# Optimization experiments

Hardware: AMD Instinct MI355X
Metric: run time of the kernel (lower is better)

Reference implementation:

```python
import jax, jax.numpy as jnp
import numpy as np

N = 100000          # active sites
C_IN = 256          # inplanes == outplanes
C_MID = 64          # innerplanes
K = 9               # 3x3 kernel offsets (2D)


def setup_inputs() -> dict:
    key = jax.random.key(0)
    ks = jax.random.split(key, 12)
    features = jax.random.normal(ks[0], (N, C_IN), dtype=jnp.float32)
    # submanifold rulebook: for each active site, index of active neighbor per
    # kernel offset; sentinel N = no active neighbor, center (offset 4) = self
    idx = jax.random.randint(ks[1], (N, K), 0, N, dtype=jnp.int32)
    drop = jax.random.uniform(ks[2], (N, K)) < 0.3
    idx = jnp.where(drop, jnp.int32(N), idx)
    neighbor_idx = idx.at[:, 4].set(jnp.arange(N, dtype=jnp.int32))
    s = 0.05
    return {
        "features": features,
        "neighbor_idx": neighbor_idx,
        "w1": jax.random.normal(ks[3], (C_IN, C_MID), dtype=jnp.float32) * s,
        "scale1": jnp.ones((C_MID,), jnp.float32),
        "bias1": jnp.zeros((C_MID,), jnp.float32),
        "w2": jax.random.normal(ks[4], (K, C_MID, C_MID), dtype=jnp.float32) * s,
        "scale2": jnp.ones((C_MID,), jnp.float32),
        "bias2": jnp.zeros((C_MID,), jnp.float32),
        "w3": jax.random.normal(ks[5], (C_MID, C_IN), dtype=jnp.float32) * s,
        "scale3": jnp.ones((C_IN,), jnp.float32),
        "bias3": jnp.zeros((C_IN,), jnp.float32),
    }


def reference(features, neighbor_idx, w1, scale1, bias1, w2, scale2, bias2,
              w3, scale3, bias3):
    # conv1: 1x1 submanifold conv == per-site matmul; affine BN; ReLU
    out = jax.nn.relu(features @ w1 * scale1 + bias1)            # [N, C_MID]
    # conv2: 3x3 submanifold conv via rulebook gather-matmul-accumulate
    padded = jnp.concatenate([out, jnp.zeros((1, C_MID), out.dtype)], axis=0)
    gathered = padded[neighbor_idx]                               # [N, K, C_MID]
    out = jnp.einsum('nkc,kcd->nd', gathered, w2)                 # [N, C_MID]
    out = jax.nn.relu(out * scale2 + bias2)
    # conv3: 1x1 conv; affine BN; residual add (downsample=None); ReLU
    out = out @ w3 * scale3 + bias3 + features                    # [N, C_IN]
    return jax.nn.relu(out)
```

## Files before the change

### kernel.cpp

```cpp
#include <hip/hip_runtime.h>
#include <stdint.h>

#define C_IN 256
#define C_MID 64
#define KOFF 9

typedef __attribute__((ext_vector_type(8))) short bf16x8;
typedef __attribute__((ext_vector_type(4))) short short4v;
typedef __attribute__((ext_vector_type(4))) float f32x4;
typedef __attribute__((ext_vector_type(4))) float float4v;

__device__ inline unsigned short f2bf(float f) {
    union { float f; unsigned u; } x; x.f = f;
    unsigned r = x.u + 0x7FFFu + ((x.u >> 16) & 1u);
    return (unsigned short)(r >> 16);
}

__global__ void prep_kernel(const float* __restrict__ w1, const float* __restrict__ s1,
                            const float* __restrict__ w2, const float* __restrict__ s2,
                            const float* __restrict__ w3, const float* __restrict__ s3,
                            unsigned short* __restrict__ w1t,
                            unsigned short* __restrict__ w2t,
                            unsigned short* __restrict__ w3t,
                            unsigned short* __restrict__ zrow) {
    int tid = blockIdx.x * blockDim.x + threadIdx.x;
    int stride = gridDim.x * blockDim.x;
    for (int i = tid; i < C_MID * C_IN; i += stride) {
        int n = i / C_IN, k = i % C_IN;
        w1t[i] = f2bf(w1[k * C_MID + n] * s1[n]);
    }
    for (int i = tid; i < KOFF * C_MID * C_MID; i += stride) {
        int k = i / (C_MID * C_MID);
        int r = i % (C_MID * C_MID);
        int d = r / C_MID, c = r % C_MID;
        w2t[i] = f2bf(w2[(k * C_MID + c) * C_MID + d] * s2[d]);
    }
    for (int i = tid; i < C_IN * C_MID; i += stride) {
        int e = i / C_MID, c = i % C_MID;
        w3t[i] = f2bf(w3[c * C_IN + e] * s3[e]);
    }
    for (int i = tid; i < C_MID; i += stride) zrow[i] = 0;
}

__global__ __launch_bounds__(256, 4) void conv1_kernel(
    const float* __restrict__ feat, const unsigned short* __restrict__ w1t,
    const float* __restrict__ b1, unsigned short* __restrict__ out1, int N)
{
    __shared__ __align__(16) unsigned short sW1[16384];

    int t = threadIdx.x;
    int wave = t >> 6;
    int lane = t & 63;
    int l15 = lane & 15;
    int quad = lane >> 4;
    int site = blockIdx.x * 64 + wave * 16 + l15;
    int sitec = site < N ? site : (N - 1);

    const bf16x8* w1c = reinterpret_cast<const bf16x8*>(w1t);
    bf16x8* sW1c = reinterpret_cast<bf16x8*>(sW1);
#pragma unroll
    for (int it = 0; it < 8; ++it) {
        int s = it * 256 + t;
        int l = s & 15, ct = (s >> 4) & 3, q = (s >> 6) & 3, kk = s >> 8;
        sW1c[s] = w1c[(ct * 16 + l) * 32 + kk * 4 + q];
    }

    float4v fr0[8];
#pragma unroll
    for (int kk = 0; kk < 4; ++kk) {
        const float4v* p = reinterpret_cast<const float4v*>(
            feat + (size_t)sitec * C_IN + kk * 32 + quad * 8);
        fr0[kk * 2] = p[0];
        fr0[kk * 2 + 1] = p[1];
    }
    __builtin_amdgcn_sched_barrier(0);
    __syncthreads();

    float4v fr1[8];
#pragma unroll
    for (int kk = 0; kk < 4; ++kk) {
        const float4v* p = reinterpret_cast<const float4v*>(
            feat + (size_t)sitec * C_IN + (kk + 4) * 32 + quad * 8);
        fr1[kk * 2] = p[0];
        fr1[kk * 2 + 1] = p[1];
    }
    __builtin_amdgcn_sched_barrier(0);

    f32x4 acc[4] = {};
#pragma unroll
    for (int kk = 0; kk < 4; ++kk) {
        union { unsigned short s[8]; bf16x8 v; } ua;
#pragma unroll
        for (int j = 0; j < 4; ++j) {
            ua.s[j] = f2bf(fr0[kk * 2][j]);
            ua.s[4 + j] = f2bf(fr0[kk * 2 + 1][j]);
        }
#pragma unroll
        for (int ct = 0; ct < 4; ++ct) {
            bf16x8 fa = sW1c[((kk * 4 + quad) * 4 + ct) * 16 + l15];
            acc[ct] = __builtin_amdgcn_mfma_f32_16x16x32_bf16(fa, ua.v, acc[ct], 0, 0, 0);
        }
    }
#pragma unroll
    for (int kk = 0; kk < 4; ++kk) {
        union { unsigned short s[8]; bf16x8 v; } ua;
#pragma unroll
        for (int j = 0; j < 4; ++j) {
            ua.s[j] = f2bf(fr1[kk * 2][j]);
            ua.s[4 + j] = f2bf(fr1[kk * 2 + 1][j]);
        }
#pragma unroll
        for (int ct = 0; ct < 4; ++ct) {
            bf16x8 fa = sW1c[(((kk + 4) * 4 + quad) * 4 + ct) * 16 + l15];
            acc[ct] = __builtin_amdgcn_mfma_f32_16x16x32_bf16(fa, ua.v, acc[ct], 0, 0, 0);
        }
    }
    if (site < N) {
#pragma unroll
        for (int ct = 0; ct < 4; ++ct) {
            float4v bb = *reinterpret_cast<const float4v*>(b1 + ct * 16 + quad * 4);
            union { unsigned short s[4]; short4v v; } o;
#pragma unroll
            for (int reg = 0; reg < 4; ++reg)
                o.s[reg] = f2bf(fmaxf(acc[ct][reg] + bb[reg], 0.f));
            *reinterpret_cast<short4v*>(out1 + (size_t)site * C_MID + ct * 16 + quad * 4) = o.v;
        }
    }
}

__global__ __launch_bounds__(256, 2) void conv23_kernel(
    const float* __restrict__ feat, const int* __restrict__ nbr,
    const unsigned short* __restrict__ out1, const unsigned short* __restrict__ w2t,
    const float* __restrict__ b2, const unsigned short* __restrict__ w3t,
    const float* __restrict__ b3, float* __restrict__ out, int N)
{
    __shared__ __align__(16) unsigned short sWB[21504];
    __shared__ int sNbr[64 * KOFF];

    int t = threadIdx.x;
    int wave = t >> 6;
    int lane = t & 63;
    int l15 = lane & 15;
    int quad = lane >> 4;
    int rt = wave * 16 + l15;
    int site = blockIdx.x * 64 + rt;
    int sitec = site < N ? site : (N - 1);

    bf16x8* sWBc = reinterpret_cast<bf16x8*>(sWB);
    const bf16x8* w2c = reinterpret_cast<const bf16x8*>(w2t);

#pragma unroll
    for (int it = 0; it < 10; ++it) {
        int s = it * 256 + t;
        int l = s & 15, ct = (s >> 4) & 3, q = (s >> 6) & 3, kk = (s >> 8) & 1, k = s >> 9;
        sWBc[s] = w2c[k * 512 + (ct * 16 + l) * 8 + kk * 4 + q];
    }
#pragma unroll
    for (int i = 0; i < 3; ++i) {
        int j = i * 256 + t;
        if (j < 64 * KOFF) {
            int g = blockIdx.x * 64 * KOFF + j;
            sNbr[j] = (g < N * KOFF) ? nbr[g] : N;
        }
    }
    __syncthreads();

    int nb[KOFF];
#pragma unroll
    for (int k = 0; k < KOFF; ++k) nb[k] = sNbr[rt * KOFF + k];

    bf16x8 ga[KOFF][2];
#pragma unroll
    for (int k = 0; k < KOFF; ++k) {
        const bf16x8* pg = reinterpret_cast<const bf16x8*>(out1 + (size_t)nb[k] * C_MID + quad * 8);
        ga[k][0] = pg[0];
        ga[k][1] = pg[4];
    }
    __builtin_amdgcn_sched_barrier(0);

    f32x4 acc2[4] = {};
#pragma unroll
    for (int k = 0; k < 5; ++k) {
#pragma unroll
        for (int kk = 0; kk < 2; ++kk) {
#pragma unroll
            for (int ct = 0; ct < 4; ++ct) {
                bf16x8 fa = sWBc[((k * 2 + kk) * 4 + quad) * 64 + ct * 16 + l15];
                acc2[ct] = __builtin_amdgcn_mfma_f32_16x16x32_bf16(fa, ga[k][kk], acc2[ct], 0, 0, 0);
            }
        }
    }
    __syncthreads();

#pragma unroll
    for (int it = 0; it < 8; ++it) {
        int s = it * 256 + t;
        int l = s & 15, ct = (s >> 4) & 3, q = (s >> 6) & 3, kk = (s >> 8) & 1, k2 = s >> 9;
        sWBc[s] = w2c[(5 + k2) * 512 + (ct * 16 + l) * 8 + kk * 4 + q];
    }
    __syncthreads();
#pragma unroll
    for (int k = 5; k < KOFF; ++k) {
        int kloc = k - 5;
#pragma unroll
        for (int kk = 0; kk < 2; ++kk) {
#pragma unroll
            for (int ct = 0; ct < 4; ++ct) {
                bf16x8 fa = sWBc[((kloc * 2 + kk) * 4 + quad) * 64 + ct * 16 + l15];
                acc2[ct] = __builtin_amdgcn_mfma_f32_16x16x32_bf16(fa, ga[k][kk], acc2[ct], 0, 0, 0);
            }
        }
    }
    float4v rf[16];
#pragma unroll
    for (int c2 = 0; c2 < 16; ++c2)
        rf[c2] = *reinterpret_cast<const float4v*>(
            feat + (size_t)sitec * C_IN + c2 * 16 + quad * 4);
    __builtin_amdgcn_sched_barrier(0);
    __syncthreads();

    unsigned short* mid = &sWB[16384];
#pragma unroll
    for (int ct = 0; ct < 4; ++ct) {
        float4v bb = *reinterpret_cast<const float4v*>(b2 + ct * 16 + quad * 4);
        union { unsigned short s[4]; short4v v; } o;
#pragma unroll
        for (int reg = 0; reg < 4; ++reg)
            o.s[reg] = f2bf(fmaxf(acc2[ct][reg] + bb[reg], 0.f));
        *reinterpret_cast<short4v*>(&mid[rt * 72 + ct * 16 + quad * 4]) = o.v;
    }
    const bf16x8* w3c = reinterpret_cast<const bf16x8*>(w3t);
#pragma unroll
    for (int it = 0; it < 8; ++it) {
        int s = it * 256 + t;
        int l = s & 15, c2 = (s >> 4) & 15, q = (s >> 8) & 3, kk = (s >> 10) & 1;
        sWBc[s] = w3c[(c2 * 16 + l) * 8 + kk * 4 + q];
    }
    __syncthreads();

    f32x4 acc3[16] = {};
#pragma unroll
    for (int kk = 0; kk < 2; ++kk) {
        bf16x8 fb = *reinterpret_cast<const bf16x8*>(
            &mid[rt * 72 + kk * 32 + quad * 8]);
#pragma unroll
        for (int c2 = 0; c2 < 16; ++c2) {
            bf16x8 fa = sWBc[((kk * 4 + quad) * 16 + c2) * 16 + l15];
            acc3[c2] = __builtin_amdgcn_mfma_f32_16x16x32_bf16(fa, fb, acc3[c2], 0, 0, 0);
        }
    }
    if (site < N) {
#pragma unroll
        for (int c2 = 0; c2 < 16; ++c2) {
            float4v bb = *reinterpret_cast<const float4v*>(b3 + c2 * 16 + quad * 4);
            float4v o;
#pragma unroll
            for (int reg = 0; reg < 4; ++reg)
                o[reg] = fmaxf(acc3[c2][reg] + bb[reg] + rf[c2][reg], 0.f);
            *reinterpret_cast<float4v*>(out + (size_t)site * C_IN + c2 * 16 + quad * 4) = o;
        }
    }
}

extern "C" void kernel_launch(void* const* d_in, const int* in_sizes, int n_in,
                              void* d_out, int out_size, void* d_ws, size_t ws_size,
                              hipStream_t stream) {
    const float* feat = (const float*)d_in[0];
    const int*   nbr  = (const int*)d_in[1];
    const float* w1   = (const float*)d_in[2];
    const float* s1   = (const float*)d_in[3];
    const float* b1   = (const float*)d_in[4];
    const float* w2   = (const float*)d_in[5];
    const float* s2   = (const float*)d_in[6];
    const float* b2   = (const float*)d_in[7];
    const float* w3   = (const float*)d_in[8];
    const float* s3   = (const float*)d_in[9];
    const float* b3   = (const float*)d_in[10];
    float* out = (float*)d_out;
    int N = in_sizes[0] / C_IN;

    char* ws = (char*)d_ws;
    unsigned short* w1t  = (unsigned short*)(ws);
    unsigned short* w2t  = (unsigned short*)(ws + 32768);
    unsigned short* w3t  = (unsigned short*)(ws + 32768 + 73728);
    unsigned short* out1 = (unsigned short*)(ws + 139264);

    prep_kernel<<<80, 256, 0, stream>>>(w1, s1, w2, s2, w3, s3, w1t, w2t, w3t,
                                        out1 + (size_t)N * C_MID);
    int nblk = (N + 63) / 64;
    conv1_kernel<<<nblk, 256, 0, stream>>>(feat, w1t, b1, out1, N);
    conv23_kernel<<<nblk, 256, 0, stream>>>(feat, nbr, out1, w2t, b2, w3t, b3, out, N);
}
```

Baseline: 260.7 us.

## Read weights directly from global/L2 instead of staging in LDS; raise conv23 occupancy

Removes the LDS weight-staging loops and their barriers in both conv1 and conv23, so each lane loads MFMA weight fragments straight from global memory, where they should hit cache. conv23 now keeps only the small mid buffer in shared memory, raises launch bounds to 4 blocks per CU, and computes the conv3 output in four chunks of four column tiles to cut accumulator registers. The aim is to drop per-block weight copy and sync overhead and gain occupancy for latency hiding. The cost is more scattered global loads per MFMA operand, which rely on L1/L2 hit rates.

```diff
diff --git a/kernel.cpp b/kernel.cpp
--- a/kernel.cpp
+++ b/kernel.cpp
@@ -46,8 +46,6 @@
     const float* __restrict__ feat, const unsigned short* __restrict__ w1t,
     const float* __restrict__ b1, unsigned short* __restrict__ out1, int N)
 {
-    __shared__ __align__(16) unsigned short sW1[16384];
-
     int t = threadIdx.x;
     int wave = t >> 6;
     int lane = t & 63;
@@ -57,61 +55,29 @@
     int sitec = site < N ? site : (N - 1);
 
     const bf16x8* w1c = reinterpret_cast<const bf16x8*>(w1t);
-    bf16x8* sW1c = reinterpret_cast<bf16x8*>(sW1);
-#pragma unroll
-    for (int it = 0; it < 8; ++it) {
-        int s = it * 256 + t;
-        int l = s & 15, ct = (s >> 4) & 3, q = (s >> 6) & 3, kk = s >> 8;
-        sW1c[s] = w1c[(ct * 16 + l) * 32 + kk * 4 + q];
-    }
-
-    float4v fr0[8];
-#pragma unroll
-    for (int kk = 0; kk < 4; ++kk) {
+
+    float4v fr[16];
+#pragma unroll
+    for (int kk = 0; kk < 8; ++kk) {
         const float4v* p = reinterpret_cast<const float4v*>(
             feat + (size_t)sitec * C_IN + kk * 32 + quad * 8);
-        fr0[kk * 2] = p[0];
-        fr0[kk * 2 + 1] = p[1];
+        fr[kk * 2] = p[0];
+        fr[kk * 2 + 1] = p[1];
     }
     __builtin_amdgcn_sched_barrier(0);
-    __syncthreads();
-
-    float4v fr1[8];
-#pragma unroll
-    for (int kk = 0; kk < 4; ++kk) {
-        const float4v* p = reinterpret_cast<const float4v*>(
-            feat + (size_t)sitec * C_IN + (kk + 4) * 32 + quad * 8);
-        fr1[kk * 2] = p[0];
-        fr1[kk * 2 + 1] = p[1];
-    }
-    __builtin_amdgcn_sched_barrier(0);
 
     f32x4 acc[4] = {};
 #pragma unroll
-    for (int kk = 0; kk < 4; ++kk) {
+    for (int kk = 0; kk < 8; ++kk) {
         union { unsigned short s[8]; bf16x8 v; } ua;
 #pragma unroll
         for (int j = 0; j < 4; ++j) {
-            ua.s[j] = f2bf(fr0[kk * 2][j]);
-            ua.s[4 + j] = f2bf(fr0[kk * 2 + 1][j]);
+            ua.s[j] = f2bf(fr[kk * 2][j]);
+            ua.s[4 + j] = f2bf(fr[kk * 2 + 1][j]);
         }
 #pragma unroll
         for (int ct = 0; ct < 4; ++ct) {
-            bf16x8 fa = sW1c[((kk * 4 + quad) * 4 + ct) * 16 + l15];
-            acc[ct] = __builtin_amdgcn_mfma_f32_16x16x32_bf16(fa, ua.v, acc[ct], 0, 0, 0);
-        }
-    }
-#pragma unroll
-    for (int kk = 0; kk < 4; ++kk) {
-        union { unsigned short s[8]; bf16x8 v; } ua;
-#pragma unroll
-        for (int j = 0; j < 4; ++j) {
-            ua.s[j] = f2bf(fr1[kk * 2][j]);
-            ua.s[4 + j] = f2bf(fr1[kk * 2 + 1][j]);
-        }
-#pragma unroll
-        for (int ct = 0; ct < 4; ++ct) {
-            bf16x8 fa = sW1c[(((kk + 4) * 4 + quad) * 4 + ct) * 16 + l15];
+            bf16x8 fa = w1c[(ct * 16 + l15) * 32 + kk * 4 + quad];
             acc[ct] = __builtin_amdgcn_mfma_f32_16x16x32_bf16(fa, ua.v, acc[ct], 0, 0, 0);
         }
     }
@@ -128,13 +94,13 @@
     }
 }
 
-__global__ __launch_bounds__(256, 2) void conv23_kernel(
+__global__ __launch_bounds__(256, 4) void conv23_kernel(
     const float* __restrict__ feat, const int* __restrict__ nbr,
     const unsigned short* __restrict__ out1, const unsigned short* __restrict__ w2t,
     const float* __restrict__ b2, const unsigned short* __restrict__ w3t,
     const float* __restrict__ b3, float* __restrict__ out, int N)
 {
-    __shared__ __align__(16) unsigned short sWB[21504];
+    __shared__ __align__(16) unsigned short mid[64 * 72];
     __shared__ int sNbr[64 * KOFF];
 
     int t = threadIdx.x;
@@ -146,15 +112,6 @@
     int site = blockIdx.x * 64 + rt;
     int sitec = site < N ? site : (N - 1);
 
-    bf16x8* sWBc = reinterpret_cast<bf16x8*>(sWB);
-    const bf16x8* w2c = reinterpret_cast<const bf16x8*>(w2t);
-
-#pragma unroll
-    for (int it = 0; it < 10; ++it) {
-        int s = it * 256 + t;
-        int l = s & 15, ct = (s >> 4) & 3, q = (s >> 6) & 3, kk = (s >> 8) & 1, k = s >> 9;
-        sWBc[s] = w2c[k * 512 + (ct * 16 + l) * 8 + kk * 4 + q];
-    }
 #pragma unroll
     for (int i = 0; i < 3; ++i) {
         int j = i * 256 + t;
@@ -178,86 +135,64 @@
     }
     __builtin_amdgcn_sched_barrier(0);
 
+    const bf16x8* w2c = reinterpret_cast<const bf16x8*>(w2t);
     f32x4 acc2[4] = {};
 #pragma unroll
-    for (int k = 0; k < 5; ++k) {
+    for (int k = 0; k < KOFF; ++k) {
 #pragma unroll
         for (int kk = 0; kk < 2; ++kk) {
 #pragma unroll
             for (int ct = 0; ct < 4; ++ct) {
-                bf16x8 fa = sWBc[((k * 2 + kk) * 4 + quad) * 64 + ct * 16 + l15];
+                bf16x8 fa = w2c[k * 512 + (ct * 16 + l15) * 8 + kk * 4 + quad];
                 acc2[ct] = __builtin_amdgcn_mfma_f32_16x16x32_bf16(fa, ga[k][kk], acc2[ct], 0, 0, 0);
             }
         }
     }
+
+#pragma unroll
+    for (int ct = 0; ct < 4; ++ct) {
+        float4v bb = *reinterpret_cast<const float4v*>(b2 + ct * 16 + quad * 4);
+        union { unsigned short s[4]; short4v v; } o;
+#pragma unroll
+        for (int reg = 0; reg < 4; ++reg)
+            o.s[reg] = f2bf(fmaxf(acc2[ct][reg] + bb[reg], 0.f));
+        *reinterpret_cast<short4v*>(&mid[rt * 72 + ct * 16 + quad * 4]) = o.v;
+    }
     __syncthreads();
 
-#pragma unroll
-    for (int it = 0; it < 8; ++it) {
-        int s = it * 256 + t;
-        int l = s & 15, ct = (s >> 4) & 3, q = (s >> 6) & 3, kk = (s >> 8) & 1, k2 = s >> 9;
-        sWBc[s] = w2c[(5 + k2) * 512 + (ct * 16 + l) * 8 + kk * 4 + q];
-    }
-    __syncthreads();
-#pragma unroll
-    for (int k = 5; k < KOFF; ++k) {
-        int kloc = k - 5;
-#pragma unroll
-        for (int kk = 0; kk < 2; ++kk) {
-#pragma unroll
-            for (int ct = 0; ct < 4; ++ct) {
-                bf16x8 fa = sWBc[((kloc * 2 + kk) * 4 + quad) * 64 + ct * 16 + l15];
-                acc2[ct] = __builtin_amdgcn_mfma_f32_16x16x32_bf16(fa, ga[k][kk], acc2[ct], 0, 0, 0);
-            }
-        }
-    }
     float4v rf[16];
 #pragma unroll
     for (int c2 = 0; c2 < 16; ++c2)
         rf[c2] = *reinterpret_cast<const float4v*>(
             feat + (size_t)sitec * C_IN + c2 * 16 + quad * 4);
     __builtin_amdgcn_sched_barrier(0);
-    __syncthreads();
-
-    unsigned short* mid = &sWB[16384];
-#pragma unroll
-    for (int ct = 0; ct < 4; ++ct) {
-        float4v bb = *reinterpret_cast<const float4v*>(b2 + ct * 16 + quad * 4);
-        union { unsigned short s[4]; short4v v; } o;
-#pragma unroll
-        for (int reg = 0; reg < 4; ++reg)
-            o.s[reg] = f2bf(fmaxf(acc2[ct][reg] + bb[reg], 0.f));
-        *reinterpret_cast<short4v*>(&mid[rt * 72 + ct * 16 + quad * 4]) = o.v;
-    }
+
     const bf16x8* w3c = reinterpret_cast<const bf16x8*>(w3t);
 #pragma unroll
-    for (int it = 0; it < 8; ++it) {
-        int s = it * 256 + t;
-        int l = s & 15, c2 = (s >> 4) & 15, q = (s >> 8) & 3, kk = (s >> 10) & 1;
-        sWBc[s] = w3c[(c2 * 16 + l) * 8 + kk * 4 + q];
-    }
-    __syncthreads();
-
-    f32x4 acc3[16] = {};
-#pragma unroll
-    for (int kk = 0; kk < 2; ++kk) {
-        bf16x8 fb = *reinterpret_cast<const bf16x8*>(
-            &mid[rt * 72 + kk * 32 + quad * 8]);
-#pragma unroll
-        for (int c2 = 0; c2 < 16; ++c2) {
-            bf16x8 fa = sWBc[((kk * 4 + quad) * 16 + c2) * 16 + l15];
-            acc3[c2] = __builtin_amdgcn_mfma_f32_16x16x32_bf16(fa, fb, acc3[c2], 0, 0, 0);
-        }
-    }
-    if (site < N) {
-#pragma unroll
-        for (int c2 = 0; c2 < 16; ++c2) {
-            float4v bb = *reinterpret_cast<const float4v*>(b3 + c2 * 16 + quad * 4);
-            float4v o;
-#pragma unroll
-            for (int reg = 0; reg < 4; ++reg)
-                o[reg] = fmaxf(acc3[c2][reg] + bb[reg] + rf[c2][reg], 0.f);
-            *reinterpret_cast<float4v*>(out + (size_t)site * C_IN + c2 * 16 + quad * 4) = o;
+    for (int c = 0; c < 4; ++c) {
+        f32x4 acc3[4] = {};
+#pragma unroll
+        for (int kk = 0; kk < 2; ++kk) {
+            bf16x8 fb = *reinterpret_cast<const bf16x8*>(
+                &mid[rt * 72 + kk * 32 + quad * 8]);
+#pragma unroll
+            for (int c2l = 0; c2l < 4; ++c2l) {
+                int c2 = c * 4 + c2l;
+                bf16x8 fa = w3c[(c2 * 16 + l15) * 8 + kk * 4 + quad];
+                acc3[c2l] = __builtin_amdgcn_mfma_f32_16x16x32_bf16(fa, fb, acc3[c2l], 0, 0, 0);
+            }
+        }
+        if (site < N) {
+#pragma unroll
+            for (int c2l = 0; c2l < 4; ++c2l) {
+                int c2 = c * 4 + c2l;
+                float4v bb = *reinterpret_cast<const float4v*>(b3 + c2 * 16 + quad * 4);
+                float4v o;
+#pragma unroll
+                for (int reg = 0; reg < 4; ++reg)
+                    o[reg] = fmaxf(acc3[c2l][reg] + bb[reg] + rf[c2][reg], 0.f);
+                *reinterpret_cast<float4v*>(out + (size_t)site * C_IN + c2 * 16 + quad * 4) = o;
+            }
         }
     }
 }
```

New measurement: 326.1 us. 25.1% more time.

## Split fused conv2/conv3 kernel into separate kernels via bf16 mid buffer

Applied to the files above, without the earlier changes.

Replaces the fused conv23 kernel with a conv2 kernel that writes the bf16 intermediate to workspace and a conv3 kernel that reads it back, when the workspace is large enough. Each kernel uses less LDS and fewer registers, so it targets higher occupancy (launch bounds of 3 blocks per CU) and better latency hiding for the gathers and the residual loads. conv2 streams its weights in three stages, and conv3 stores its output in chunks of four tiles to cut live accumulators. The cost is an extra global round trip for the mid tensor (about 12.8MB written and read) plus one more kernel launch.

```diff
diff --git a/kernel.cpp b/kernel.cpp
--- a/kernel.cpp
+++ b/kernel.cpp
@@ -128,6 +128,180 @@
     }
 }
 
+__global__ __launch_bounds__(256, 3) void conv2_kernel(
+    const int* __restrict__ nbr, const unsigned short* __restrict__ out1,
+    const unsigned short* __restrict__ w2t, const float* __restrict__ b2,
+    unsigned short* __restrict__ mid, int N)
+{
+    __shared__ __align__(16) unsigned short sW2[12288];
+    __shared__ int sNbr[64 * KOFF];
+
+    int t = threadIdx.x;
+    int wave = t >> 6;
+    int lane = t & 63;
+    int l15 = lane & 15;
+    int quad = lane >> 4;
+    int rt = wave * 16 + l15;
+    int site = blockIdx.x * 64 + rt;
+
+    bf16x8* sW2c = reinterpret_cast<bf16x8*>(sW2);
+    const bf16x8* w2c = reinterpret_cast<const bf16x8*>(w2t);
+
+#pragma unroll
+    for (int it = 0; it < 6; ++it) {
+        int s = it * 256 + t;
+        int l = s & 15, ct = (s >> 4) & 3, q = (s >> 6) & 3, kk = (s >> 8) & 1, k2 = s >> 9;
+        sW2c[s] = w2c[k2 * 512 + (ct * 16 + l) * 8 + kk * 4 + q];
+    }
+#pragma unroll
+    for (int i = 0; i < 3; ++i) {
+        int j = i * 256 + t;
+        if (j < 64 * KOFF) {
+            int g = blockIdx.x * 64 * KOFF + j;
+            sNbr[j] = (g < N * KOFF) ? nbr[g] : N;
+        }
+    }
+    __syncthreads();
+
+    int nb[KOFF];
+#pragma unroll
+    for (int k = 0; k < KOFF; ++k) nb[k] = sNbr[rt * KOFF + k];
+
+    bf16x8 ga[KOFF][2];
+#pragma unroll
+    for (int k = 0; k < KOFF; ++k) {
+        const bf16x8* pg = reinterpret_cast<const bf16x8*>(out1 + (size_t)nb[k] * C_MID + quad * 8);
+        ga[k][0] = pg[0];
+        ga[k][1] = pg[4];
+    }
+    __builtin_amdgcn_sched_barrier(0);
+
+    f32x4 acc2[4] = {};
+#pragma unroll
+    for (int k2 = 0; k2 < 3; ++k2) {
+#pragma unroll
+        for (int kk = 0; kk < 2; ++kk) {
+#pragma unroll
+            for (int ct = 0; ct < 4; ++ct) {
+                bf16x8 fa = sW2c[((k2 * 2 + kk) * 4 + quad) * 64 + ct * 16 + l15];
+                acc2[ct] = __builtin_amdgcn_mfma_f32_16x16x32_bf16(fa, ga[k2][kk], acc2[ct], 0, 0, 0);
+            }
+        }
+    }
+    __syncthreads();
+
+#pragma unroll
+    for (int it = 0; it < 6; ++it) {
+        int s = it * 256 + t;
+        int l = s & 15, ct = (s >> 4) & 3, q = (s >> 6) & 3, kk = (s >> 8) & 1, k2 = s >> 9;
+        sW2c[s] = w2c[(3 + k2) * 512 + (ct * 16 + l) * 8 + kk * 4 + q];
+    }
+    __syncthreads();
+#pragma unroll
+    for (int k2 = 0; k2 < 3; ++k2) {
+#pragma unroll
+        for (int kk = 0; kk < 2; ++kk) {
+#pragma unroll
+            for (int ct = 0; ct < 4; ++ct) {
+                bf16x8 fa = sW2c[((k2 * 2 + kk) * 4 + quad) * 64 + ct * 16 + l15];
+                acc2[ct] = __builtin_amdgcn_mfma_f32_16x16x32_bf16(fa, ga[3 + k2][kk], acc2[ct], 0, 0, 0);
+            }
+        }
+    }
+    __syncthreads();
+
+#pragma unroll
+    for (int it = 0; it < 6; ++it) {
+        int s = it * 256 + t;
+        int l = s & 15, ct = (s >> 4) & 3, q = (s >> 6) & 3, kk = (s >> 8) & 1, k2 = s >> 9;
+        sW2c[s] = w2c[(6 + k2) * 512 + (ct * 16 + l) * 8 + kk * 4 + q];
+    }
+    __syncthreads();
+#pragma unroll
+    for (int k2 = 0; k2 < 3; ++k2) {
+#pragma unroll
+        for (int kk = 0; kk < 2; ++kk) {
+#pragma unroll
+            for (int ct = 0; ct < 4; ++ct) {
+                bf16x8 fa = sW2c[((k2 * 2 + kk) * 4 + quad) * 64 + ct * 16 + l15];
+                acc2[ct] = __builtin_amdgcn_mfma_f32_16x16x32_bf16(fa, ga[6 + k2][kk], acc2[ct], 0, 0, 0);
+            }
+        }
+    }
+
+    if (site < N) {
+#pragma unroll
+        for (int ct = 0; ct < 4; ++ct) {
+            float4v bb = *reinterpret_cast<const float4v*>(b2 + ct * 16 + quad * 4);
+            union { unsigned short s[4]; short4v v; } o;
+#pragma unroll
+            for (int reg = 0; reg < 4; ++reg)
+                o.s[reg] = f2bf(fmaxf(acc2[ct][reg] + bb[reg], 0.f));
+            *reinterpret_cast<short4v*>(mid + (size_t)site * C_MID + ct * 16 + quad * 4) = o.v;
+        }
+    }
+}
+
+__global__ __launch_bounds__(256, 3) void conv3_kernel(
+    const float* __restrict__ feat, const unsigned short* __restrict__ mid,
+    const unsigned short* __restrict__ w3t, const float* __restrict__ b3,
+    float* __restrict__ out, int N)
+{
+    __shared__ __align__(16) unsigned short sW3[16384];
+
+    int t = threadIdx.x;
+    int wave = t >> 6;
+    int lane = t & 63;
+    int l15 = lane & 15;
+    int quad = lane >> 4;
+    int site = blockIdx.x * 64 + wave * 16 + l15;
+    int sitec = site < N ? site : (N - 1);
+
+    bf16x8* sW3c = reinterpret_cast<bf16x8*>(sW3);
+    const bf16x8* w3c = reinterpret_cast<const bf16x8*>(w3t);
+#pragma unroll
+    for (int it = 0; it < 8; ++it) {
+        int s = it * 256 + t;
+        int l = s & 15, c2 = (s >> 4) & 15, q = (s >> 8) & 3, kk = (s >> 10) & 1;
+        sW3c[s] = w3c[(c2 * 16 + l) * 8 + kk * 4 + q];
+    }
+
+    bf16x8 fb0 = *reinterpret_cast<const bf16x8*>(mid + (size_t)sitec * C_MID + quad * 8);
+    bf16x8 fb1 = *reinterpret_cast<const bf16x8*>(mid + (size_t)sitec * C_MID + 32 + quad * 8);
+    float4v rf[16];
+#pragma unroll
+    for (int c2 = 0; c2 < 16; ++c2)
+        rf[c2] = *reinterpret_cast<const float4v*>(
+            feat + (size_t)sitec * C_IN + c2 * 16 + quad * 4);
+    __builtin_amdgcn_sched_barrier(0);
+    __syncthreads();
+
+#pragma unroll
+    for (int c = 0; c < 4; ++c) {
+        f32x4 acc3[4] = {};
+#pragma unroll
+        for (int c2l = 0; c2l < 4; ++c2l) {
+            int c2 = c * 4 + c2l;
+            bf16x8 fa0 = sW3c[((0 * 4 + quad) * 16 + c2) * 16 + l15];
+            acc3[c2l] = __builtin_amdgcn_mfma_f32_16x16x32_bf16(fa0, fb0, acc3[c2l], 0, 0, 0);
+            bf16x8 fa1 = sW3c[((1 * 4 + quad) * 16 + c2) * 16 + l15];
+            acc3[c2l] = __builtin_amdgcn_mfma_f32_16x16x32_bf16(fa1, fb1, acc3[c2l], 0, 0, 0);
+        }
+        if (site < N) {
+#pragma unroll
+            for (int c2l = 0; c2l < 4; ++c2l) {
+                int c2 = c * 4 + c2l;
+                float4v bb = *reinterpret_cast<const float4v*>(b3 + c2 * 16 + quad * 4);
+                float4v o;
+#pragma unroll
+                for (int reg = 0; reg < 4; ++reg)
+                    o[reg] = fmaxf(acc3[c2l][reg] + bb[reg] + rf[c2][reg], 0.f);
+                *reinterpret_cast<float4v*>(out + (size_t)site * C_IN + c2 * 16 + quad * 4) = o;
+            }
+        }
+    }
+}
+
 __global__ __launch_bounds__(256, 2) void conv23_kernel(
     const float* __restrict__ feat, const int* __restrict__ nbr,
     const unsigned short* __restrict__ out1, const unsigned short* __restrict__ w2t,
@@ -219,7 +393,7 @@
     __builtin_amdgcn_sched_barrier(0);
     __syncthreads();
 
-    unsigned short* mid = &sWB[16384];
+    unsigned short* midl = &sWB[16384];
 #pragma unroll
     for (int ct = 0; ct < 4; ++ct) {
         float4v bb = *reinterpret_cast<const float4v*>(b2 + ct * 16 + quad * 4);
@@ -227,7 +401,7 @@
 #pragma unroll
         for (int reg = 0; reg < 4; ++reg)
             o.s[reg] = f2bf(fmaxf(acc2[ct][reg] + bb[reg], 0.f));
-        *reinterpret_cast<short4v*>(&mid[rt * 72 + ct * 16 + quad * 4]) = o.v;
+        *reinterpret_cast<short4v*>(&midl[rt * 72 + ct * 16 + quad * 4]) = o.v;
     }
     const bf16x8* w3c = reinterpret_cast<const bf16x8*>(w3t);
 #pragma unroll
@@ -242,7 +416,7 @@
 #pragma unroll
     for (int kk = 0; kk < 2; ++kk) {
         bf16x8 fb = *reinterpret_cast<const bf16x8*>(
-            &mid[rt * 72 + kk * 32 + quad * 8]);
+            &midl[rt * 72 + kk * 32 + quad * 8]);
 #pragma unroll
         for (int c2 = 0; c2 < 16; ++c2) {
             bf16x8 fa = sWBc[((kk * 4 + quad) * 16 + c2) * 16 + l15];
@@ -285,9 +459,19 @@
     unsigned short* w3t  = (unsigned short*)(ws + 32768 + 73728);
     unsigned short* out1 = (unsigned short*)(ws + 139264);
 
+    size_t out1_bytes = (size_t)(N + 1) * C_MID * 2;
+    size_t need_split = 139264 + out1_bytes + (size_t)N * C_MID * 2;
+
     prep_kernel<<<80, 256, 0, stream>>>(w1, s1, w2, s2, w3, s3, w1t, w2t, w3t,
                                         out1 + (size_t)N * C_MID);
     int nblk = (N + 63) / 64;
     conv1_kernel<<<nblk, 256, 0, stream>>>(feat, w1t, b1, out1, N);
-    conv23_kernel<<<nblk, 256, 0, stream>>>(feat, nbr, out1, w2t, b2, w3t, b3, out, N);
-}
+
+    if (ws_size >= need_split) {
+        unsigned short* mid = (unsigned short*)(ws + 139264 + out1_bytes);
+        conv2_kernel<<<nblk, 256, 0, stream>>>(nbr, out1, w2t, b2, mid, N);
+        conv3_kernel<<<nblk, 256, 0, stream>>>(feat, mid, w3t, b3, out, N);
+    } else {
+        conv23_kernel<<<nblk, 256, 0, stream>>>(feat, nbr, out1, w2t, b2, w3t, b3, out, N);
+    }
+}
```

Result: slower. 266.7 us (+2.3%).

## Shrink conv23 LDS footprint to fit three blocks per CU

Applied to the files above, without the earlier changes.

Splits the w2 weight staging into three phases of three offsets, so the shared buffer shrinks from about 43KB to about 35KB with a separate mid buffer. The w3 operands are now read directly from global memory (L2-cached) instead of being staged in LDS. The conv3 output is produced in four column chunks of four accumulators each, which cuts live registers. Together with launch_bounds(256,3) this aims to raise occupancy and hide gather latency, at the cost of extra barriers and global weight loads per wave.

```diff
diff --git a/kernel.cpp b/kernel.cpp
--- a/kernel.cpp
+++ b/kernel.cpp
@@ -128,13 +128,14 @@
     }
 }
 
-__global__ __launch_bounds__(256, 2) void conv23_kernel(
+__global__ __launch_bounds__(256, 3) void conv23_kernel(
     const float* __restrict__ feat, const int* __restrict__ nbr,
     const unsigned short* __restrict__ out1, const unsigned short* __restrict__ w2t,
     const float* __restrict__ b2, const unsigned short* __restrict__ w3t,
     const float* __restrict__ b3, float* __restrict__ out, int N)
 {
-    __shared__ __align__(16) unsigned short sWB[21504];
+    __shared__ __align__(16) unsigned short sW2[12288];
+    __shared__ __align__(16) unsigned short sMid[64 * 72];
     __shared__ int sNbr[64 * KOFF];
 
     int t = threadIdx.x;
@@ -146,14 +147,14 @@
     int site = blockIdx.x * 64 + rt;
     int sitec = site < N ? site : (N - 1);
 
-    bf16x8* sWBc = reinterpret_cast<bf16x8*>(sWB);
+    bf16x8* sW2c = reinterpret_cast<bf16x8*>(sW2);
     const bf16x8* w2c = reinterpret_cast<const bf16x8*>(w2t);
 
 #pragma unroll
-    for (int it = 0; it < 10; ++it) {
+    for (int it = 0; it < 6; ++it) {
         int s = it * 256 + t;
-        int l = s & 15, ct = (s >> 4) & 3, q = (s >> 6) & 3, kk = (s >> 8) & 1, k = s >> 9;
-        sWBc[s] = w2c[k * 512 + (ct * 16 + l) * 8 + kk * 4 + q];
+        int l = s & 15, ct = (s >> 4) & 3, q = (s >> 6) & 3, kk = (s >> 8) & 1, k2 = s >> 9;
+        sW2c[s] = w2c[k2 * 512 + (ct * 16 + l) * 8 + kk * 4 + q];
     }
 #pragma unroll
     for (int i = 0; i < 3; ++i) {
@@ -180,37 +181,67 @@
 
     f32x4 acc2[4] = {};
 #pragma unroll
-    for (int k = 0; k < 5; ++k) {
+    for (int k2 = 0; k2 < 3; ++k2) {
 #pragma unroll
         for (int kk = 0; kk < 2; ++kk) {
 #pragma unroll
             for (int ct = 0; ct < 4; ++ct) {
-                bf16x8 fa = sWBc[((k * 2 + kk) * 4 + quad) * 64 + ct * 16 + l15];
-                acc2[ct] = __builtin_amdgcn_mfma_f32_16x16x32_bf16(fa, ga[k][kk], acc2[ct], 0, 0, 0);
+                bf16x8 fa = sW2c[((k2 * 2 + kk) * 4 + quad) * 64 + ct * 16 + l15];
+                acc2[ct] = __builtin_amdgcn_mfma_f32_16x16x32_bf16(fa, ga[k2][kk], acc2[ct], 0, 0, 0);
             }
         }
     }
     __syncthreads();
 
 #pragma unroll
-    for (int it = 0; it < 8; ++it) {
+    for (int it = 0; it < 6; ++it) {
         int s = it * 256 + t;
         int l = s & 15, ct = (s >> 4) & 3, q = (s >> 6) & 3, kk = (s >> 8) & 1, k2 = s >> 9;
-        sWBc[s] = w2c[(5 + k2) * 512 + (ct * 16 + l) * 8 + kk * 4 + q];
-    }
-    __syncthreads();
-#pragma unroll
-    for (int k = 5; k < KOFF; ++k) {
-        int kloc = k - 5;
+        sW2c[s] = w2c[(3 + k2) * 512 + (ct * 16 + l) * 8 + kk * 4 + q];
+    }
+    __syncthreads();
+#pragma unroll
+    for (int k2 = 0; k2 < 3; ++k2) {
 #pragma unroll
         for (int kk = 0; kk < 2; ++kk) {
 #pragma unroll
             for (int ct = 0; ct < 4; ++ct) {
-                bf16x8 fa = sWBc[((kloc * 2 + kk) * 4 + quad) * 64 + ct * 16 + l15];
-                acc2[ct] = __builtin_amdgcn_mfma_f32_16x16x32_bf16(fa, ga[k][kk], acc2[ct], 0, 0, 0);
+                bf16x8 fa = sW2c[((k2 * 2 + kk) * 4 + quad) * 64 + ct * 16 + l15];
+                acc2[ct] = __builtin_amdgcn_mfma_f32_16x16x32_bf16(fa, ga[3 + k2][kk], acc2[ct], 0, 0, 0);
             }
         }
     }
+    __syncthreads();
+
+#pragma unroll
+    for (int it = 0; it < 6; ++it) {
+        int s = it * 256 + t;
+        int l = s & 15, ct = (s >> 4) & 3, q = (s >> 6) & 3, kk = (s >> 8) & 1, k2 = s >> 9;
+        sW2c[s] = w2c[(6 + k2) * 512 + (ct * 16 + l) * 8 + kk * 4 + q];
+    }
+    __syncthreads();
+#pragma unroll
+    for (int k2 = 0; k2 < 3; ++k2) {
+#pragma unroll
+        for (int kk = 0; kk < 2; ++kk) {
+#pragma unroll
+            for (int ct = 0; ct < 4; ++ct) {
+                bf16x8 fa = sW2c[((k2 * 2 + kk) * 4 + quad) * 64 + ct * 16 + l15];
+                acc2[ct] = __builtin_amdgcn_mfma_f32_16x16x32_bf16(fa, ga[6 + k2][kk], acc2[ct], 0, 0, 0);
+            }
+        }
+    }
+
+#pragma unroll
+    for (int ct = 0; ct < 4; ++ct) {
+        float4v bb = *reinterpret_cast<const float4v*>(b2 + ct * 16 + quad * 4);
+        union { unsigned short s[4]; short4v v; } o;
+#pragma unroll
+        for (int reg = 0; reg < 4; ++reg)
+            o.s[reg] = f2bf(fmaxf(acc2[ct][reg] + bb[reg], 0.f));
+        *reinterpret_cast<short4v*>(&sMid[rt * 72 + ct * 16 + quad * 4]) = o.v;
+    }
+
     float4v rf[16];
 #pragma unroll
     for (int c2 = 0; c2 < 16; ++c2)
@@ -219,45 +250,32 @@
     __builtin_amdgcn_sched_barrier(0);
     __syncthreads();
 
-    unsigned short* mid = &sWB[16384];
-#pragma unroll
-    for (int ct = 0; ct < 4; ++ct) {
-        float4v bb = *reinterpret_cast<const float4v*>(b2 + ct * 16 + quad * 4);
-        union { unsigned short s[4]; short4v v; } o;
-#pragma unroll
-        for (int reg = 0; reg < 4; ++reg)
-            o.s[reg] = f2bf(fmaxf(acc2[ct][reg] + bb[reg], 0.f));
-        *reinterpret_cast<short4v*>(&mid[rt * 72 + ct * 16 + quad * 4]) = o.v;
-    }
+    bf16x8 fb0 = *reinterpret_cast<const bf16x8*>(&sMid[rt * 72 + quad * 8]);
+    bf16x8 fb1 = *reinterpret_cast<const bf16x8*>(&sMid[rt * 72 + 32 + quad * 8]);
+
     const bf16x8* w3c = reinterpret_cast<const bf16x8*>(w3t);
 #pragma unroll
-    for (int it = 0; it < 8; ++it) {
-        int s = it * 256 + t;
-        int l = s & 15, c2 = (s >> 4) & 15, q = (s >> 8) & 3, kk = (s >> 10) & 1;
-        sWBc[s] = w3c[(c2 * 16 + l) * 8 + kk * 4 + q];
-    }
-    __syncthreads();
-
-    f32x4 acc3[16] = {};
-#pragma unroll
-    for (int kk = 0; kk < 2; ++kk) {
-        bf16x8 fb = *reinterpret_cast<const bf16x8*>(
-            &mid[rt * 72 + kk * 32 + quad * 8]);
-#pragma unroll
-        for (int c2 = 0; c2 < 16; ++c2) {
-            bf16x8 fa = sWBc[((kk * 4 + quad) * 16 + c2) * 16 + l15];
-            acc3[c2] = __builtin_amdgcn_mfma_f32_16x16x32_bf16(fa, fb, acc3[c2], 0, 0, 0);
-        }
-    }
-    if (site < N) {
-#pragma unroll
-        for (int c2 = 0; c2 < 16; ++c2) {
-            float4v bb = *reinterpret_cast<const float4v*>(b3 + c2 * 16 + quad * 4);
-            float4v o;
-#pragma unroll
-            for (int reg = 0; reg < 4; ++reg)
-                o[reg] = fmaxf(acc3[c2][reg] + bb[reg] + rf[c2][reg], 0.f);
-            *reinterpret_cast<float4v*>(out + (size_t)site * C_IN + c2 * 16 + quad * 4) = o;
+    for (int c = 0; c < 4; ++c) {
+        f32x4 acc3[4] = {};
+#pragma unroll
+        for (int c2l = 0; c2l < 4; ++c2l) {
+            int c2 = c * 4 + c2l;
+            bf16x8 fa0 = w3c[(c2 * 16 + l15) * 8 + quad];
+            acc3[c2l] = __builtin_amdgcn_mfma_f32_16x16x32_bf16(fa0, fb0, acc3[c2l], 0, 0, 0);
+            bf16x8 fa1 = w3c[(c2 * 16 + l15) * 8 + 4 + quad];
+            acc3[c2l] = __builtin_amdgcn_mfma_f32_16x16x32_bf16(fa1, fb1, acc3[c2l], 0, 0, 0);
+        }
+        if (site < N) {
+#pragma unroll
+            for (int c2l = 0; c2l < 4; ++c2l) {
+                int c2 = c * 4 + c2l;
+                float4v bb = *reinterpret_cast<const float4v*>(b3 + c2 * 16 + quad * 4);
+                float4v o;
+#pragma unroll
+                for (int reg = 0; reg < 4; ++reg)
+                    o[reg] = fmaxf(acc3[c2l][reg] + bb[reg] + rf[c2][reg], 0.f);
+                *reinterpret_cast<float4v*>(out + (size_t)site * C_IN + c2 * 16 + quad * 4) = o;
+            }
         }
     }
 }
```

Measured after the change: 273.3 us. 1.05x slower.
